# Kernel optimization log

Hardware: AMD Instinct MI355X
Metric: run time of the kernel (lower is better)

The kernel has to match this reference:

```python
import jax, jax.numpy as jnp
import numpy as np

TEMP = 0.07
BASE_TEMP = 0.07
EPS = 1e-8


def setup_inputs() -> dict:
    key = jax.random.key(0)
    features = jax.random.normal(key, (4096, 2, 128), dtype=jnp.float32)
    return {"features": features}


def reference(features):
    B, V, D = features.shape  # bsz, n_views, dim
    # torch.cat(torch.unbind(features, dim=1), dim=0): view-major ordering
    cf = jnp.swapaxes(features, 0, 1).reshape(V * B, D)  # [N, D], N = V*B
    # cosine similarity = normalize rows then GEMM (same math as broadcasted CosineSimilarity)
    n = cf / jnp.maximum(jnp.linalg.norm(cf, axis=-1, keepdims=True), EPS)
    logits = jnp.matmul(n, n.T) / TEMP  # [N, N]
    N = V * B
    logits_mask = 1.0 - jnp.eye(N, dtype=logits.dtype)  # zero out self-contrast
    # SimCLR mask: eye(B) tiled over (anchor_count, contrast_count), minus diagonal
    pos_mask = jnp.tile(jnp.eye(B, dtype=logits.dtype), (V, V)) * logits_mask
    exp_logits = jnp.exp(logits) * logits_mask
    log_prob = logits - jnp.log(exp_logits.sum(axis=1, keepdims=True))
    mean_log_prob_pos = (pos_mask * log_prob).sum(axis=1) / pos_mask.sum(axis=1)
    loss = -(TEMP / BASE_TEMP) * mean_log_prob_pos
    return loss.reshape(V, B).mean()
```

## Files before the change

### kernel.cpp

```cpp
#include <hip/hip_runtime.h>
#include <hip/hip_bf16.h>
#include <math.h>


constexpr int   Bsz   = 4096;
constexpr int   Nrows = 8192;
constexpr int   Dd    = 128;
constexpr float TEMPf = 0.07f;
constexpr float EPSN  = 1e-8f;
constexpr float SCALE = 1.4426950408889634f / 0.07f;
constexpr float LN2   = 0.6931471805599453f;

constexpr int CHUNKS     = 32;
constexpr int CHUNK_COLS = Nrows / CHUNKS;
constexpr int STEPS      = 4;
constexpr int ROWS_BLK   = 256;
constexpr int NPAIRS     = CHUNKS * (CHUNKS + 1) / 2;
constexpr int YG         = Nrows / ROWS_BLK;
constexpr int PREPBLKS   = Bsz / 4;

typedef __attribute__((ext_vector_type(8)))  short bf16x8;
typedef __attribute__((ext_vector_type(16))) float floatx16;


constexpr size_t OFF_PART = 0x200000;
constexpr size_t OFF_SPOS = 0x300000;

__device__ __forceinline__ void gld_lds16(const void* g, void* l) {
    __builtin_amdgcn_global_load_lds(
        (const __attribute__((address_space(1))) void*)g,
        (__attribute__((address_space(3))) void*)l, 16, 0, 0);
}

__global__ void prep_k(const float* __restrict__ f,
                       char* __restrict__ nF,
                       float* __restrict__ sposPart,
                       float* __restrict__ out) {
    __shared__ float sred[4];
    int tid  = threadIdx.x;
    int wid  = tid >> 6;
    int lane = tid & 63;
    int b    = blockIdx.x * 4 + wid;
    if (blockIdx.x == 0 && tid == 0) out[0] = 0.f;

    const float* s0 = f + (size_t)(b * 2) * Dd;
    float2 x = *(const float2*)(s0 + lane * 2);
    float2 y = *(const float2*)(s0 + Dd + lane * 2);
    float ss0 = x.x * x.x + x.y * x.y;
    float ss1 = y.x * y.x + y.y * y.y;
    float dt  = x.x * y.x + x.y * y.y;
    #pragma unroll
    for (int off = 32; off; off >>= 1) {
        ss0 += __shfl_xor(ss0, off);
        ss1 += __shfl_xor(ss1, off);
        dt  += __shfl_xor(dt,  off);
    }
    float inv0 = 1.0f / fmaxf(sqrtf(ss0), EPSN);
    float inv1 = 1.0f / fmaxf(sqrtf(ss1), EPSN);

    size_t poff = (size_t)(lane >> 3) * 1024 + ((lane >> 2) & 1) * 512
                + (lane & 3) * 4;

    __hip_bfloat162 h;
    h.x = __float2bfloat16(x.x * inv0);
    h.y = __float2bfloat16(x.y * inv0);
    *(__hip_bfloat162*)(nF + (size_t)(b >> 5) * 8192 + (b & 31) * 16 + poff) = h;
    int r1 = Bsz + b;
    h.x = __float2bfloat16(y.x * inv1);
    h.y = __float2bfloat16(y.y * inv1);
    *(__hip_bfloat162*)(nF + (size_t)(r1 >> 5) * 8192 + (r1 & 31) * 16 + poff) = h;

    if (lane == 0) sred[wid] = dt * inv0 * inv1 / TEMPf;
    __syncthreads();
    if (tid == 0) sposPart[blockIdx.x] = sred[0] + sred[1] + sred[2] + sred[3];
}

__global__ __launch_bounds__(256, 3)
void main_k(const char* __restrict__ nF, float* __restrict__ partial) {
    __shared__ char  bufs[2][16384];
    __shared__ float colred[4][256];
    __shared__ float rred[256];
    const int tid  = threadIdx.x;
    const int wid  = tid >> 6;
    const int lane = tid & 63;
    const int lo   = lane & 31;
    const int hi   = lane >> 5;

    int p = blockIdx.x, ci = 0;
    while (p >= CHUNKS - ci) { p -= CHUNKS - ci; ci++; }
    const int cj = ci + p;

    const int rbase = ci * ROWS_BLK + wid * 64;
    const int cbase = cj * ROWS_BLK;
    const int cg0   = cj * 8;

    bf16x8 afrag[2][8];
    #pragma unroll
    for (int g = 0; g < 2; g++) {
        const char* ag = nF + (size_t)((rbase + g * 32) >> 5) * 8192 + lane * 16;
        #pragma unroll
        for (int kc = 0; kc < 8; kc++)
            afrag[g][kc] = *(const bf16x8*)(ag + kc * 1024);
    }

    float rs[2][16];
    #pragma unroll
    for (int g = 0; g < 2; g++)
        #pragma unroll
        for (int r = 0; r < 16; r++) rs[g][r] = 0.f;

    {
        const char* g0 = nF + (size_t)cg0 * 8192;
        int kc = wid * 2;
        gld_lds16(g0 + kc * 1024 + lane * 16,              &bufs[0][kc * 1024]);
        gld_lds16(g0 + (kc + 1) * 1024 + lane * 16,        &bufs[0][(kc + 1) * 1024]);
        gld_lds16(g0 + 8192 + kc * 1024 + lane * 16,       &bufs[0][8192 + kc * 1024]);
        gld_lds16(g0 + 8192 + (kc + 1) * 1024 + lane * 16, &bufs[0][8192 + (kc + 1) * 1024]);
    }

    #pragma unroll 1
    for (int st = 0; st < STEPS; st++) {
        __syncthreads();
        if (st + 1 < STEPS) {
            const char* gn = nF + (size_t)(cg0 + 2 * (st + 1)) * 8192;
            char* dst = bufs[(st + 1) & 1];
            int kc = wid * 2;
            gld_lds16(gn + kc * 1024 + lane * 16,              dst + kc * 1024);
            gld_lds16(gn + (kc + 1) * 1024 + lane * 16,        dst + (kc + 1) * 1024);
            gld_lds16(gn + 8192 + kc * 1024 + lane * 16,       dst + 8192 + kc * 1024);
            gld_lds16(gn + 8192 + (kc + 1) * 1024 + lane * 16, dst + 8192 + (kc + 1) * 1024);
        }

        const char* buf = bufs[st & 1];
        #pragma unroll
        for (int u = 0; u < 2; u++) {
            floatx16 acc0 = {}, acc1 = {};
            #pragma unroll
            for (int kc = 0; kc < 8; kc++) {
                bf16x8 bf = *(const bf16x8*)&buf[u * 8192 + kc * 1024 + lane * 16];
                acc0 = __builtin_amdgcn_mfma_f32_32x32x16_bf16(afrag[0][kc], bf, acc0, 0, 0, 0);
                acc1 = __builtin_amdgcn_mfma_f32_32x32x16_bf16(afrag[1][kc], bf, acc1, 0, 0, 0);
            }

            const int tt   = st * 2 + u;
            const int cb32 = cbase + tt * 32;
            float cs = 0.f;
            #pragma unroll
            for (int g = 0; g < 2; g++) {
                const floatx16& acc = g ? acc1 : acc0;
                if (cb32 == rbase + g * 32) {
                    #pragma unroll
                    for (int r = 0; r < 16; r++) {
                        float e = __builtin_amdgcn_exp2f(acc[r] * SCALE);
                        if (lo == ((r & 3) + 8 * (r >> 2) + 4 * hi)) e = 0.f;
                        cs += e; rs[g][r] += e;
                    }
                } else {
                    #pragma unroll
                    for (int r = 0; r < 16; r++) {
                        float e = __builtin_amdgcn_exp2f(acc[r] * SCALE);
                        cs += e; rs[g][r] += e;
                    }
                }
            }
            cs += __shfl_xor(cs, 32);
            if (hi == 0) colred[wid][tt * 32 + lo] = cs;
        }
    }

    if (ci != cj) {
        #pragma unroll
        for (int g = 0; g < 2; g++) {
            #pragma unroll
            for (int r = 0; r < 16; r++) {
                float v = rs[g][r];
                v += __shfl_xor(v, 1);
                v += __shfl_xor(v, 2);
                v += __shfl_xor(v, 4);
                v += __shfl_xor(v, 8);
                v += __shfl_xor(v, 16);
                if (lo == r)
                    rred[wid * 64 + g * 32 + ((r & 3) + 8 * (r >> 2) + 4 * hi)] = v;
            }
        }
    }

    __syncthreads();
    float v = colred[0][tid] + colred[1][tid] + colred[2][tid] + colred[3][tid];
    partial[(size_t)ci * Nrows + cbase + tid] = v;
    if (ci != cj)
        partial[(size_t)cj * Nrows + ci * ROWS_BLK + tid] = rred[tid];
}

__global__ __launch_bounds__(256)
void final_k(const float* __restrict__ partial, const float* __restrict__ sposPart,
             float* __restrict__ out) {
    __shared__ float red[4];
    int tid = threadIdx.x;
    int r = blockIdx.x * 256 + tid;
    float se = 0.f;
    #pragma unroll
    for (int p = 0; p < YG; p++) se += partial[(size_t)p * Nrows + r];
    float acc = __builtin_amdgcn_logf(se) * LN2;
    if (tid < 32) acc -= 2.f * sposPart[blockIdx.x * 32 + tid];
    #pragma unroll
    for (int off = 32; off; off >>= 1) acc += __shfl_xor(acc, off);
    if ((tid & 63) == 0) red[tid >> 6] = acc;
    __syncthreads();
    if (tid == 0)
        atomicAdd(out, (red[0] + red[1] + red[2] + red[3]) / (float)Nrows);
}

extern "C" void kernel_launch(void* const* d_in, const int* in_sizes, int n_in,
                              void* d_out, int out_size, void* d_ws, size_t ws_size,
                              hipStream_t stream) {
    const float* f = (const float*)d_in[0];
    char* ws = (char*)d_ws;
    char* nF        = ws;
    float* partial  = (float*)(ws + OFF_PART);
    float* sposPart = (float*)(ws + OFF_SPOS);

    prep_k<<<PREPBLKS, 256, 0, stream>>>(f, nF, sposPart, (float*)d_out);
    main_k<<<NPAIRS, 256, 0, stream>>>(nF, partial);
    final_k<<<Nrows / 256, 256, 0, stream>>>(partial, sposPart, (float*)d_out);
}
```

Baseline: 89.90 us.

## Use triple-buffered 32-column LDS tiles with vmcnt-based waits

New measurement: 124.5 us. 1.38x slower.

```diff
diff --git a/kernel.cpp b/kernel.cpp
--- a/kernel.cpp
+++ b/kernel.cpp
@@ -13,7 +13,7 @@
 
 constexpr int CHUNKS     = 32;
 constexpr int CHUNK_COLS = Nrows / CHUNKS;
-constexpr int STEPS      = 4;
+constexpr int TILES      = CHUNK_COLS / 32;
 constexpr int ROWS_BLK   = 256;
 constexpr int NPAIRS     = CHUNKS * (CHUNKS + 1) / 2;
 constexpr int YG         = Nrows / ROWS_BLK;
@@ -77,7 +77,9 @@
 
 __global__ __launch_bounds__(256, 3)
 void main_k(const char* __restrict__ nF, float* __restrict__ partial) {
-    __shared__ char  bufs[2][16384];
+    __shared__ char  buf0[8192];
+    __shared__ char  buf1[8192];
+    __shared__ char  buf2[8192];
     __shared__ float colred[4][256];
     __shared__ float rred[256];
     const int tid  = threadIdx.x;
@@ -109,63 +111,58 @@
         #pragma unroll
         for (int r = 0; r < 16; r++) rs[g][r] = 0.f;
 
-    {
-        const char* g0 = nF + (size_t)cg0 * 8192;
+    char* const bufp[3] = {buf0, buf1, buf2};
+
+    auto stage = [&](char* dst, int cg) {
+        const char* g = nF + (size_t)cg * 8192;
         int kc = wid * 2;
-        gld_lds16(g0 + kc * 1024 + lane * 16,              &bufs[0][kc * 1024]);
-        gld_lds16(g0 + (kc + 1) * 1024 + lane * 16,        &bufs[0][(kc + 1) * 1024]);
-        gld_lds16(g0 + 8192 + kc * 1024 + lane * 16,       &bufs[0][8192 + kc * 1024]);
-        gld_lds16(g0 + 8192 + (kc + 1) * 1024 + lane * 16, &bufs[0][8192 + (kc + 1) * 1024]);
-    }
-
-    #pragma unroll 1
-    for (int st = 0; st < STEPS; st++) {
-        __syncthreads();
-        if (st + 1 < STEPS) {
-            const char* gn = nF + (size_t)(cg0 + 2 * (st + 1)) * 8192;
-            char* dst = bufs[(st + 1) & 1];
-            int kc = wid * 2;
-            gld_lds16(gn + kc * 1024 + lane * 16,              dst + kc * 1024);
-            gld_lds16(gn + (kc + 1) * 1024 + lane * 16,        dst + (kc + 1) * 1024);
-            gld_lds16(gn + 8192 + kc * 1024 + lane * 16,       dst + 8192 + kc * 1024);
-            gld_lds16(gn + 8192 + (kc + 1) * 1024 + lane * 16, dst + 8192 + (kc + 1) * 1024);
+        gld_lds16(g + kc * 1024 + lane * 16,       dst + kc * 1024);
+        gld_lds16(g + (kc + 1) * 1024 + lane * 16, dst + (kc + 1) * 1024);
+    };
+
+    auto compute = [&](const char* buf, int t) {
+        floatx16 acc0 = {}, acc1 = {};
+        #pragma unroll
+        for (int kc = 0; kc < 8; kc++) {
+            bf16x8 bf = *(const bf16x8*)&buf[kc * 1024 + lane * 16];
+            acc0 = __builtin_amdgcn_mfma_f32_32x32x16_bf16(afrag[0][kc], bf, acc0, 0, 0, 0);
+            acc1 = __builtin_amdgcn_mfma_f32_32x32x16_bf16(afrag[1][kc], bf, acc1, 0, 0, 0);
         }
-
-        const char* buf = bufs[st & 1];
-        #pragma unroll
-        for (int u = 0; u < 2; u++) {
-            floatx16 acc0 = {}, acc1 = {};
-            #pragma unroll
-            for (int kc = 0; kc < 8; kc++) {
-                bf16x8 bf = *(const bf16x8*)&buf[u * 8192 + kc * 1024 + lane * 16];
-                acc0 = __builtin_amdgcn_mfma_f32_32x32x16_bf16(afrag[0][kc], bf, acc0, 0, 0, 0);
-                acc1 = __builtin_amdgcn_mfma_f32_32x32x16_bf16(afrag[1][kc], bf, acc1, 0, 0, 0);
-            }
-
-            const int tt   = st * 2 + u;
-            const int cb32 = cbase + tt * 32;
-            float cs = 0.f;
-            #pragma unroll
-            for (int g = 0; g < 2; g++) {
-                const floatx16& acc = g ? acc1 : acc0;
-                if (cb32 == rbase + g * 32) {
-                    #pragma unroll
-                    for (int r = 0; r < 16; r++) {
-                        float e = __builtin_amdgcn_exp2f(acc[r] * SCALE);
-                        if (lo == ((r & 3) + 8 * (r >> 2) + 4 * hi)) e = 0.f;
-                        cs += e; rs[g][r] += e;
-                    }
-                } else {
-                    #pragma unroll
-                    for (int r = 0; r < 16; r++) {
-                        float e = __builtin_amdgcn_exp2f(acc[r] * SCALE);
-                        cs += e; rs[g][r] += e;
-                    }
+        const int cb32 = cbase + t * 32;
+        float cs = 0.f;
+        #pragma unroll
+        for (int g = 0; g < 2; g++) {
+            const floatx16& acc = g ? acc1 : acc0;
+            if (cb32 == rbase + g * 32) {
+                #pragma unroll
+                for (int r = 0; r < 16; r++) {
+                    float e = __builtin_amdgcn_exp2f(acc[r] * SCALE);
+                    if (lo == ((r & 3) + 8 * (r >> 2) + 4 * hi)) e = 0.f;
+                    cs += e; rs[g][r] += e;
+                }
+            } else {
+                #pragma unroll
+                for (int r = 0; r < 16; r++) {
+                    float e = __builtin_amdgcn_exp2f(acc[r] * SCALE);
+                    cs += e; rs[g][r] += e;
                 }
             }
-            cs += __shfl_xor(cs, 32);
-            if (hi == 0) colred[wid][tt * 32 + lo] = cs;
         }
+        cs += __shfl_xor(cs, 32);
+        if (hi == 0) colred[wid][t * 32 + lo] = cs;
+    };
+
+    stage(buf0, cg0 + 0);
+    stage(buf1, cg0 + 1);
+
+    #pragma unroll
+    for (int t = 0; t < TILES; t++) {
+        if (t < TILES - 1) __builtin_amdgcn_s_waitcnt(0xF72);
+        else               __builtin_amdgcn_s_waitcnt(0xF70);
+        __builtin_amdgcn_s_barrier();
+        __builtin_amdgcn_sched_barrier(0);
+        if (t + 2 < TILES) stage(bufp[(t + 2) % 3], cg0 + t + 2);
+        compute(bufp[t % 3], t);
     }
 
     if (ci != cj) {
```
